# Kernel tuning notes

Measured on AMD Instinct MI355X. Metric: run time of the kernel, lower is better.

## Reference

```python
import jax, jax.numpy as jnp
import numpy as np

N, T = 2000, 8
INFEAT, HID, OUT, H = 32, 16, 32, 4
ALPHA = 0.2
D1 = HID * H   # 64, layer-1 GRU dim (concat heads)
D2 = OUT       # 32, layer-2 GRU dim (mean heads)
NEG = -1e9


def setup_inputs() -> dict:
    key = jax.random.key(0)
    ks = jax.random.split(key, 12)
    xav = lambda k, shape, fi, fo: (jax.random.normal(k, shape, dtype=jnp.float32)
                                    * np.float32(np.sqrt(2.0 / (fi + fo))))
    # sparse-ish binary adjacency with self loops, per timestep
    A = (jax.random.uniform(ks[0], (T, N, N)) < 0.01).astype(jnp.float32)
    A = jnp.maximum(A, jnp.eye(N, dtype=jnp.float32)[None])
    feats = jax.random.normal(ks[1], (T, N, INFEAT), dtype=jnp.float32) * 0.1
    return {
        "A": A,
        "feats": feats,
        "gat1_W": xav(ks[2], (H, INFEAT, HID), INFEAT, HID),
        "gat1_a": xav(ks[3], (H, 2, HID), 2 * HID, 1),
        "gru1_W": xav(ks[4], (3, N, D1, D1), D1, D1),
        "gru1_U": xav(ks[5], (3, N, D1, D1), D1, D1),
        "gru1_b": jnp.zeros((3, N, D1), jnp.float32),
        "q1": xav(ks[6], (N, D1), N, D1),   # GAT_init_features, layer 1
        "gat2_W": xav(ks[7], (H, D1, OUT), D1, OUT),
        "gat2_a": xav(ks[8], (H, 2, OUT), 2 * OUT, 1),
        "gru2_W": xav(ks[9], (3, N, D2, D2), D2, D2),
        "gru2_U": xav(ks[10], (3, N, D2, D2), D2, D2),
        "gru2_b": jnp.zeros((3, N, D2), jnp.float32),
        "q2": xav(ks[11], (N, D2), N, D2),  # GAT_init_features, layer 2
    }


def _gat(x, At, W, a, concat):
    # x: [N,F], At: [N,N], W: [H,F,D], a: [H,2,D]
    h = jnp.einsum('nf,hfd->hnd', x, W)                       # [H,N,D]
    e_src = jnp.einsum('hnd,hd->hn', h, a[:, 0])              # [H,N]
    e_dst = jnp.einsum('hnd,hd->hn', h, a[:, 1])
    e = jax.nn.leaky_relu(e_src[:, :, None] + e_dst[:, None, :], ALPHA)
    e = jnp.where(At[None] > 0, e, NEG)
    att = jax.nn.softmax(e, axis=-1)                          # [H,N,N]
    o = jnp.einsum('hnm,hmd->hnd', att, h)
    if concat:
        return jax.nn.elu(o).transpose(1, 0, 2).reshape(x.shape[0], -1)  # [N,H*D]
    return o.mean(axis=0)                                     # [N,D]


def _gru_step(Q, Z, Wg, Ug, bg):
    # batched per-node mat_GRU_cell: Wg/Ug [3,N,D,D], bg [3,N,D]; gates: update, reset, htilda
    wz = jnp.einsum('gnij,nj->gni', Wg, Z) + bg               # [3,N,D]
    upd = jax.nn.sigmoid(wz[0] + jnp.einsum('nij,nj->ni', Ug[0], Q))
    rst = jax.nn.sigmoid(wz[1] + jnp.einsum('nij,nj->ni', Ug[1], Q))
    hcap = jnp.tanh(wz[2] + jnp.einsum('nij,nj->ni', Ug[2], rst * Q))
    return (1.0 - upd) * Q + upd * hcap


def _grcu_layer(A, feats, q0, W, a, Wg, Ug, bg, concat):
    def step(Q, inp):
        At, xt = inp
        Z = _gat(xt, At, W, a, concat)
        Qn = _gru_step(Q, Z, Wg, Ug, bg)
        return Qn, Qn
    _, seq = jax.lax.scan(step, q0, (A, feats))
    return seq  # [T,N,Dim]


def reference(A, feats, gat1_W, gat1_a, gru1_W, gru1_U, gru1_b, q1,
              gat2_W, gat2_a, gru2_W, gru2_U, gru2_b, q2):
    s1 = _grcu_layer(A, feats, q1, gat1_W, gat1_a, gru1_W, gru1_U, gru1_b, True)
    s2 = _grcu_layer(A, s1, q2, gat2_W, gat2_a, gru2_W, gru2_U, gru2_b, False)
    return s2.reshape(-1, s2.shape[-1])  # torch.cat(out_seq, dim=0) -> [T*N, OUT]
```

## Files before the change

kernel.cpp:

```cpp
#include <hip/hip_runtime.h>
#include <cstdint>
#include <cstddef>

#define NNODES 2000
#define TSTEPS 8
#define NHEADS 4
#define CAP    96
#define NROWS  (TSTEPS * NNODES)

__global__ void k1_csr_gath1(const float* __restrict__ A,
                             int* __restrict__ nbr, int* __restrict__ cnt,
                             const float* __restrict__ feats,
                             const float* __restrict__ W, const float* __restrict__ a,
                             float* __restrict__ hbuf, float* __restrict__ es,
                             float* __restrict__ ed) {
    const int lane = threadIdx.x;
    if (blockIdx.x < NROWS) {
        const int row = blockIdx.x;
        const float4* Ar4 = reinterpret_cast<const float4*>(A + (size_t)row * NNODES);
        int* outp = nbr + (size_t)row * CAP;
        const unsigned long long lmask = (1ull << lane) - 1ull;
        int c = 0;
        for (int j4 = lane; j4 < NNODES / 4; j4 += 64) {
            float4 v = Ar4[j4];
            #pragma unroll
            for (int cc = 0; cc < 4; ++cc) {
                float x = (cc == 0) ? v.x : (cc == 1) ? v.y : (cc == 2) ? v.z : v.w;
                bool p = x > 0.0f;
                unsigned long long m = __ballot(p);
                int off = __popcll(m & lmask);
                if (p && c + off < CAP) outp[c + off] = j4 * 4 + cc;
                c += (int)__popcll(m);
            }
        }
        if (lane == 0) cnt[row] = (c > CAP ? CAP : c);
    } else {
        const int b = blockIdx.x - NROWS;
        const int t = b / NNODES, n = b % NNODES;
        constexpr int F = 32, D = 16;
        const int h = lane / D, d = lane % D;
        const float* xr = feats + (size_t)b * F;
        const float* Wp = W + (size_t)h * F * D + d;
        float acc = 0.f;
        #pragma unroll
        for (int f = 0; f < F; ++f) acc += xr[f] * Wp[f * D];
        hbuf[(((size_t)t * NHEADS + h) * NNODES + n) * D + d] = acc;
        float s0 = acc * a[(h * 2 + 0) * D + d];
        float s1 = acc * a[(h * 2 + 1) * D + d];
        #pragma unroll
        for (int s = D / 2; s > 0; s >>= 1) {
            s0 += __shfl_down(s0, s, D);
            s1 += __shfl_down(s1, s, D);
        }
        if (d == 0) {
            es[((size_t)t * NHEADS + h) * NNODES + n] = s0;
            ed[((size_t)t * NHEADS + h) * NNODES + n] = s1;
        }
    }
}

template<int F, int D>
__global__ void gat_h_all_kernel(const float* __restrict__ x, const float* __restrict__ W,
                                 const float* __restrict__ a, float* __restrict__ hbuf,
                                 float* __restrict__ es, float* __restrict__ ed) {
    const int b = blockIdx.x;
    const int t = b / NNODES, n = b % NNODES;
    const int tid = threadIdx.x;
    const int h = tid / D, d = tid % D;
    const float* xr = x + (size_t)b * F;
    const float* Wp = W + (size_t)h * F * D + d;
    float acc = 0.f;
    #pragma unroll
    for (int f = 0; f < F; ++f) acc += xr[f] * Wp[f * D];
    hbuf[(((size_t)t * NHEADS + h) * NNODES + n) * D + d] = acc;
    float s0 = acc * a[(h * 2 + 0) * D + d];
    float s1 = acc * a[(h * 2 + 1) * D + d];
    #pragma unroll
    for (int s = D / 2; s > 0; s >>= 1) {
        s0 += __shfl_down(s0, s, D);
        s1 += __shfl_down(s1, s, D);
    }
    if (d == 0) {
        es[((size_t)t * NHEADS + h) * NNODES + n] = s0;
        ed[((size_t)t * NHEADS + h) * NNODES + n] = s1;
    }
}

template<int D, bool CONCAT>
__global__ void gat_attn_all_kernel(const int* __restrict__ nbr, const int* __restrict__ cnt_arr,
                                    const float* __restrict__ hbuf, const float* __restrict__ es,
                                    const float* __restrict__ ed, float* __restrict__ Z) {
    const int b = blockIdx.x;
    const int t = b / NNODES, n = b % NNODES;
    const int tid = threadIdx.x;
    const int h = tid / D, d = tid % D;
    const int cnt = cnt_arr[b];
    const int* idx = nbr + (size_t)b * CAP;
    const float* esb = es + (size_t)t * NHEADS * NNODES;
    const float* edb = ed + (size_t)t * NHEADS * NNODES;
    const float* hb  = hbuf + (size_t)t * NHEADS * NNODES * D;
    __shared__ int mlist[CAP];
    __shared__ float eds[NHEADS][CAP];
    for (int k = tid; k < cnt; k += NHEADS * D) mlist[k] = idx[k];
    __syncthreads();
    for (int k = d; k < cnt; k += D) eds[h][k] = edb[(size_t)h * NNODES + mlist[k]];
    __syncthreads();
    const float esv = esb[(size_t)h * NNODES + n];
    float maxv = -1e30f;
    for (int k = 0; k < cnt; ++k) {
        float v = esv + eds[h][k];
        v = v > 0.f ? v : 0.2f * v;
        maxv = fmaxf(maxv, v);
    }
    float wsum = 0.f, acc = 0.f;
    for (int k = 0; k < cnt; ++k) {
        float v = esv + eds[h][k];
        v = v > 0.f ? v : 0.2f * v;
        float w = __expf(v - maxv);
        wsum += w;
        acc += w * hb[((size_t)h * NNODES + mlist[k]) * D + d];
    }
    float o = acc / wsum;
    if constexpr (CONCAT) {
        float e = o > 0.f ? o : (__expf(o) - 1.0f);
        Z[(size_t)b * (NHEADS * D) + h * D + d] = e;
    } else {
        __shared__ float red[NHEADS][D];
        red[h][d] = o;
        __syncthreads();
        if (h == 0) Z[(size_t)b * D + d] =
            (red[0][d] + red[1][d] + red[2][d] + red[3][d]) * 0.25f;
    }
}

template<int D>
__global__ __launch_bounds__((D / 16) * D, 1)
void wzgru_kernel(const float* __restrict__ Wg, const float* __restrict__ Ug,
                  const float* __restrict__ bg, const float* __restrict__ Z,
                  const float* __restrict__ q0, float* __restrict__ outp) {
    constexpr int QUADS = D / 16;
    constexpr int TPB = QUADS * D;
    constexpr int F4R = D / 4;
    const int n = blockIdx.x, tid = threadIdx.x;
    const int quad = tid & (QUADS - 1);
    const int row  = tid / QUADS;
    const int cbase = quad * 16;
    __shared__ float Zs[TSTEPS][D];
    __shared__ float Qs[D], rq[D];

    for (int idx = tid; idx < TSTEPS * F4R; idx += TPB) {
        int t = idx / F4R, i4 = idx % F4R;
        reinterpret_cast<float4*>(&Zs[t][0])[i4] =
            reinterpret_cast<const float4*>(Z + ((size_t)t * NNODES + n) * D)[i4];
    }
    if (tid < D) Qs[tid] = q0[(size_t)n * D + tid];
    float bgv[3];
    #pragma unroll
    for (int g = 0; g < 3; ++g) bgv[g] = bg[((size_t)g * NNODES + n) * D + row];

    float wseg[3][16], useg[3][16];
    #pragma unroll
    for (int g = 0; g < 3; ++g) {
        const float4* W4 = reinterpret_cast<const float4*>(
            Wg + ((size_t)g * NNODES + n) * D * D + (size_t)row * D + cbase);
        #pragma unroll
        for (int c = 0; c < 4; ++c) {
            float4 v = W4[c];
            wseg[g][c * 4 + 0] = v.x; wseg[g][c * 4 + 1] = v.y;
            wseg[g][c * 4 + 2] = v.z; wseg[g][c * 4 + 3] = v.w;
        }
    }
    #pragma unroll
    for (int g = 0; g < 3; ++g) {
        const float4* U4 = reinterpret_cast<const float4*>(
            Ug + ((size_t)g * NNODES + n) * D * D + (size_t)row * D + cbase);
        #pragma unroll
        for (int c = 0; c < 4; ++c) {
            float4 v = U4[c];
            useg[g][c * 4 + 0] = v.x; useg[g][c * 4 + 1] = v.y;
            useg[g][c * 4 + 2] = v.z; useg[g][c * 4 + 3] = v.w;
        }
    }
    __syncthreads();

    float wzr[3][TSTEPS];
    #pragma unroll
    for (int t = 0; t < TSTEPS; ++t) {
        float z16[16];
        #pragma unroll
        for (int c = 0; c < 4; ++c) {
            float4 v = reinterpret_cast<const float4*>(&Zs[t][cbase])[c];
            z16[c * 4 + 0] = v.x; z16[c * 4 + 1] = v.y;
            z16[c * 4 + 2] = v.z; z16[c * 4 + 3] = v.w;
        }
        #pragma unroll
        for (int g = 0; g < 3; ++g) {
            float p = 0.f;
            #pragma unroll
            for (int c = 0; c < 16; ++c) p += wseg[g][c] * z16[c];
            if constexpr (QUADS == 4) { p += __shfl_xor(p, 1, 4); p += __shfl_xor(p, 2, 4); }
            else                      { p += __shfl_xor(p, 1, 2); }
            wzr[g][t] = p + bgv[g];
        }
    }

    #pragma unroll
    for (int t = 0; t < TSTEPS; ++t) {
        float q16[16];
        #pragma unroll
        for (int c = 0; c < 4; ++c) {
            float4 v = reinterpret_cast<const float4*>(&Qs[cbase])[c];
            q16[c * 4 + 0] = v.x; q16[c * 4 + 1] = v.y;
            q16[c * 4 + 2] = v.z; q16[c * 4 + 3] = v.w;
        }
        float p0 = 0.f, p1 = 0.f;
        #pragma unroll
        for (int c = 0; c < 16; ++c) { p0 += useg[0][c] * q16[c]; p1 += useg[1][c] * q16[c]; }
        if constexpr (QUADS == 4) {
            p0 += __shfl_xor(p0, 1, 4); p0 += __shfl_xor(p0, 2, 4);
            p1 += __shfl_xor(p1, 1, 4); p1 += __shfl_xor(p1, 2, 4);
        } else {
            p0 += __shfl_xor(p0, 1, 2); p1 += __shfl_xor(p1, 1, 2);
        }
        const float qrow = Qs[row];
        const float zg = 1.f / (1.f + __expf(-(wzr[0][t] + p0)));
        const float rg = 1.f / (1.f + __expf(-(wzr[1][t] + p1)));
        if (quad == 0) rq[row] = rg * qrow;
        __syncthreads();
        float p2 = 0.f;
        {
            float r16[16];
            #pragma unroll
            for (int c = 0; c < 4; ++c) {
                float4 v = reinterpret_cast<const float4*>(&rq[cbase])[c];
                r16[c * 4 + 0] = v.x; r16[c * 4 + 1] = v.y;
                r16[c * 4 + 2] = v.z; r16[c * 4 + 3] = v.w;
            }
            #pragma unroll
            for (int c = 0; c < 16; ++c) p2 += useg[2][c] * r16[c];
        }
        if constexpr (QUADS == 4) { p2 += __shfl_xor(p2, 1, 4); p2 += __shfl_xor(p2, 2, 4); }
        else                      { p2 += __shfl_xor(p2, 1, 2); }
        const float hcap = tanhf(wzr[2][t] + p2);
        const float qn = (1.f - zg) * qrow + zg * hcap;
        if (quad == 0) {
            Qs[row] = qn;
            outp[((size_t)t * NNODES + n) * D + row] = qn;
        }
        __syncthreads();
    }
}

extern "C" void kernel_launch(void* const* d_in, const int* in_sizes, int n_in,
                              void* d_out, int out_size, void* d_ws, size_t ws_size,
                              hipStream_t stream) {
    const float* A      = (const float*)d_in[0];
    const float* feats  = (const float*)d_in[1];
    const float* gat1_W = (const float*)d_in[2];
    const float* gat1_a = (const float*)d_in[3];
    const float* gru1_W = (const float*)d_in[4];
    const float* gru1_U = (const float*)d_in[5];
    const float* gru1_b = (const float*)d_in[6];
    const float* q1     = (const float*)d_in[7];
    const float* gat2_W = (const float*)d_in[8];
    const float* gat2_a = (const float*)d_in[9];
    const float* gru2_W = (const float*)d_in[10];
    const float* gru2_U = (const float*)d_in[11];
    const float* gru2_b = (const float*)d_in[12];
    const float* q2     = (const float*)d_in[13];
    float* out = (float*)d_out;

    char* ws = (char*)d_ws;
    int*   nbr  = (int*)ws;    ws += (size_t)NROWS * CAP * 4;
    int*   cnt  = (int*)ws;    ws += (size_t)NROWS * 4;
    float* h1   = (float*)ws;  ws += (size_t)TSTEPS * NHEADS * NNODES * 16 * 4;
    float* es1  = (float*)ws;  ws += (size_t)TSTEPS * NHEADS * NNODES * 4;
    float* ed1  = (float*)ws;  ws += (size_t)TSTEPS * NHEADS * NNODES * 4;
    float* Z1   = (float*)ws;  ws += (size_t)TSTEPS * NNODES * 64 * 4;
    float* s1   = (float*)ws;  ws += (size_t)TSTEPS * NNODES * 64 * 4;
    float* h2   = (float*)ws;  ws += (size_t)TSTEPS * NHEADS * NNODES * 32 * 4;
    float* es2  = (float*)ws;  ws += (size_t)TSTEPS * NHEADS * NNODES * 4;
    float* ed2  = (float*)ws;  ws += (size_t)TSTEPS * NHEADS * NNODES * 4;
    float* Z2   = (float*)ws;  ws += (size_t)TSTEPS * NNODES * 32 * 4;

    k1_csr_gath1<<<2 * NROWS, 64, 0, stream>>>(A, nbr, cnt, feats, gat1_W, gat1_a,
                                               h1, es1, ed1);
    gat_attn_all_kernel<16, true><<<NROWS, 64, 0, stream>>>(nbr, cnt, h1, es1, ed1, Z1);
    wzgru_kernel<64><<<NNODES, 256, 0, stream>>>(gru1_W, gru1_U, gru1_b, Z1, q1, s1);
    gat_h_all_kernel<64, 32><<<NROWS, 128, 0, stream>>>(s1, gat2_W, gat2_a, h2, es2, ed2);
    gat_attn_all_kernel<32, false><<<NROWS, 128, 0, stream>>>(nbr, cnt, h2, es2, ed2, Z2);
    wzgru_kernel<32><<<NNODES, 64, 0, stream>>>(gru2_W, gru2_U, gru2_b, Z2, q2, out);
}
```

Baseline: 173.9 us.

## Fuse layer-1 GRU with layer-2 GAT feature projection into one kernel

The layer-1 GRU kernel now also keeps each node's hidden states for all timesteps in shared memory. It then computes the layer-2 GAT projection h2 and the attention scores es2/ed2 directly from them. This removes the s1 intermediate buffer round-trip through global memory and one kernel launch of 16000 blocks. In exchange the fused kernel holds the W2 slice in more registers, and its projection work runs over only 2000 blocks of 256 threads.

New measurement: 166.3 us. 1.05x faster.

```diff
diff --git a/kernel.cpp b/kernel.cpp
--- a/kernel.cpp
+++ b/kernel.cpp
@@ -56,33 +56,6 @@
             es[((size_t)t * NHEADS + h) * NNODES + n] = s0;
             ed[((size_t)t * NHEADS + h) * NNODES + n] = s1;
         }
-    }
-}
-
-template<int F, int D>
-__global__ void gat_h_all_kernel(const float* __restrict__ x, const float* __restrict__ W,
-                                 const float* __restrict__ a, float* __restrict__ hbuf,
-                                 float* __restrict__ es, float* __restrict__ ed) {
-    const int b = blockIdx.x;
-    const int t = b / NNODES, n = b % NNODES;
-    const int tid = threadIdx.x;
-    const int h = tid / D, d = tid % D;
-    const float* xr = x + (size_t)b * F;
-    const float* Wp = W + (size_t)h * F * D + d;
-    float acc = 0.f;
-    #pragma unroll
-    for (int f = 0; f < F; ++f) acc += xr[f] * Wp[f * D];
-    hbuf[(((size_t)t * NHEADS + h) * NNODES + n) * D + d] = acc;
-    float s0 = acc * a[(h * 2 + 0) * D + d];
-    float s1 = acc * a[(h * 2 + 1) * D + d];
-    #pragma unroll
-    for (int s = D / 2; s > 0; s >>= 1) {
-        s0 += __shfl_down(s0, s, D);
-        s1 += __shfl_down(s1, s, D);
-    }
-    if (d == 0) {
-        es[((size_t)t * NHEADS + h) * NNODES + n] = s0;
-        ed[((size_t)t * NHEADS + h) * NNODES + n] = s1;
     }
 }
 
@@ -133,6 +106,152 @@
     }
 }
 
+__global__ __launch_bounds__(256, 1)
+void wzgru1_gath2_kernel(const float* __restrict__ Wg, const float* __restrict__ Ug,
+                         const float* __restrict__ bg, const float* __restrict__ Z,
+                         const float* __restrict__ q0,
+                         const float* __restrict__ W2, const float* __restrict__ a2,
+                         float* __restrict__ h2, float* __restrict__ es2,
+                         float* __restrict__ ed2) {
+    constexpr int D = 64;
+    constexpr int QUADS = 4;
+    constexpr int TPB = 256;
+    constexpr int F4R = D / 4;
+    const int n = blockIdx.x, tid = threadIdx.x;
+    const int quad = tid & (QUADS - 1);
+    const int row  = tid / QUADS;
+    const int cbase = quad * 16;
+    __shared__ float Zs[TSTEPS][D];
+    __shared__ float Qh[TSTEPS][D];
+    __shared__ float Qs[D], rq[D];
+
+    for (int idx = tid; idx < TSTEPS * F4R; idx += TPB) {
+        int t = idx / F4R, i4 = idx % F4R;
+        reinterpret_cast<float4*>(&Zs[t][0])[i4] =
+            reinterpret_cast<const float4*>(Z + ((size_t)t * NNODES + n) * D)[i4];
+    }
+    if (tid < D) Qs[tid] = q0[(size_t)n * D + tid];
+    float bgv[3];
+    #pragma unroll
+    for (int g = 0; g < 3; ++g) bgv[g] = bg[((size_t)g * NNODES + n) * D + row];
+
+    float wseg[3][16], useg[3][16];
+    #pragma unroll
+    for (int g = 0; g < 3; ++g) {
+        const float4* W4 = reinterpret_cast<const float4*>(
+            Wg + ((size_t)g * NNODES + n) * D * D + (size_t)row * D + cbase);
+        #pragma unroll
+        for (int c = 0; c < 4; ++c) {
+            float4 v = W4[c];
+            wseg[g][c * 4 + 0] = v.x; wseg[g][c * 4 + 1] = v.y;
+            wseg[g][c * 4 + 2] = v.z; wseg[g][c * 4 + 3] = v.w;
+        }
+    }
+    #pragma unroll
+    for (int g = 0; g < 3; ++g) {
+        const float4* U4 = reinterpret_cast<const float4*>(
+            Ug + ((size_t)g * NNODES + n) * D * D + (size_t)row * D + cbase);
+        #pragma unroll
+        for (int c = 0; c < 4; ++c) {
+            float4 v = U4[c];
+            useg[g][c * 4 + 0] = v.x; useg[g][c * 4 + 1] = v.y;
+            useg[g][c * 4 + 2] = v.z; useg[g][c * 4 + 3] = v.w;
+        }
+    }
+    __syncthreads();
+
+    float wzr[3][TSTEPS];
+    #pragma unroll
+    for (int t = 0; t < TSTEPS; ++t) {
+        float z16[16];
+        #pragma unroll
+        for (int c = 0; c < 4; ++c) {
+            float4 v = reinterpret_cast<const float4*>(&Zs[t][cbase])[c];
+            z16[c * 4 + 0] = v.x; z16[c * 4 + 1] = v.y;
+            z16[c * 4 + 2] = v.z; z16[c * 4 + 3] = v.w;
+        }
+        #pragma unroll
+        for (int g = 0; g < 3; ++g) {
+            float p = 0.f;
+            #pragma unroll
+            for (int c = 0; c < 16; ++c) p += wseg[g][c] * z16[c];
+            p += __shfl_xor(p, 1, 4); p += __shfl_xor(p, 2, 4);
+            wzr[g][t] = p + bgv[g];
+        }
+    }
+
+    #pragma unroll
+    for (int t = 0; t < TSTEPS; ++t) {
+        float q16[16];
+        #pragma unroll
+        for (int c = 0; c < 4; ++c) {
+            float4 v = reinterpret_cast<const float4*>(&Qs[cbase])[c];
+            q16[c * 4 + 0] = v.x; q16[c * 4 + 1] = v.y;
+            q16[c * 4 + 2] = v.z; q16[c * 4 + 3] = v.w;
+        }
+        float p0 = 0.f, p1 = 0.f;
+        #pragma unroll
+        for (int c = 0; c < 16; ++c) { p0 += useg[0][c] * q16[c]; p1 += useg[1][c] * q16[c]; }
+        p0 += __shfl_xor(p0, 1, 4); p0 += __shfl_xor(p0, 2, 4);
+        p1 += __shfl_xor(p1, 1, 4); p1 += __shfl_xor(p1, 2, 4);
+        const float qrow = Qs[row];
+        const float zg = 1.f / (1.f + __expf(-(wzr[0][t] + p0)));
+        const float rg = 1.f / (1.f + __expf(-(wzr[1][t] + p1)));
+        if (quad == 0) rq[row] = rg * qrow;
+        __syncthreads();
+        float p2 = 0.f;
+        {
+            float r16[16];
+            #pragma unroll
+            for (int c = 0; c < 4; ++c) {
+                float4 v = reinterpret_cast<const float4*>(&rq[cbase])[c];
+                r16[c * 4 + 0] = v.x; r16[c * 4 + 1] = v.y;
+                r16[c * 4 + 2] = v.z; r16[c * 4 + 3] = v.w;
+            }
+            #pragma unroll
+            for (int c = 0; c < 16; ++c) p2 += useg[2][c] * r16[c];
+        }
+        p2 += __shfl_xor(p2, 1, 4); p2 += __shfl_xor(p2, 2, 4);
+        const float hcap = tanhf(wzr[2][t] + p2);
+        const float qn = (1.f - zg) * qrow + zg * hcap;
+        if (quad == 0) {
+            Qs[row] = qn;
+            Qh[t][row] = qn;
+        }
+        __syncthreads();
+    }
+
+    const int lane = tid & 63;
+    const int hh = tid >> 6;
+    const int d2 = lane >> 1;
+    const int fh = lane & 1;
+    float w2seg[32];
+    const float* W2p = W2 + ((size_t)hh * 64 + fh * 32) * 32 + d2;
+    #pragma unroll
+    for (int j = 0; j < 32; ++j) w2seg[j] = W2p[(size_t)j * 32];
+    const float a0 = a2[(hh * 2 + 0) * 32 + d2];
+    const float a1 = a2[(hh * 2 + 1) * 32 + d2];
+    #pragma unroll
+    for (int t = 0; t < TSTEPS; ++t) {
+        float p = 0.f;
+        #pragma unroll
+        for (int j = 0; j < 32; ++j) p += w2seg[j] * Qh[t][fh * 32 + j];
+        p += __shfl_xor(p, 1, 64);
+        if (fh == 0) h2[(((size_t)t * NHEADS + hh) * NNODES + n) * 32 + d2] = p;
+        float e0 = (fh == 0) ? p * a0 : 0.f;
+        float e1 = (fh == 0) ? p * a1 : 0.f;
+        #pragma unroll
+        for (int s = 2; s <= 32; s <<= 1) {
+            e0 += __shfl_xor(e0, s, 64);
+            e1 += __shfl_xor(e1, s, 64);
+        }
+        if (lane == 0) {
+            es2[((size_t)t * NHEADS + hh) * NNODES + n] = e0;
+            ed2[((size_t)t * NHEADS + hh) * NNODES + n] = e1;
+        }
+    }
+}
+
 template<int D>
 __global__ __launch_bounds__((D / 16) * D, 1)
 void wzgru_kernel(const float* __restrict__ Wg, const float* __restrict__ Ug,
@@ -277,7 +396,6 @@
     float* es1  = (float*)ws;  ws += (size_t)TSTEPS * NHEADS * NNODES * 4;
     float* ed1  = (float*)ws;  ws += (size_t)TSTEPS * NHEADS * NNODES * 4;
     float* Z1   = (float*)ws;  ws += (size_t)TSTEPS * NNODES * 64 * 4;
-    float* s1   = (float*)ws;  ws += (size_t)TSTEPS * NNODES * 64 * 4;
     float* h2   = (float*)ws;  ws += (size_t)TSTEPS * NHEADS * NNODES * 32 * 4;
     float* es2  = (float*)ws;  ws += (size_t)TSTEPS * NHEADS * NNODES * 4;
     float* ed2  = (float*)ws;  ws += (size_t)TSTEPS * NHEADS * NNODES * 4;
@@ -286,8 +404,8 @@
     k1_csr_gath1<<<2 * NROWS, 64, 0, stream>>>(A, nbr, cnt, feats, gat1_W, gat1_a,
                                                h1, es1, ed1);
     gat_attn_all_kernel<16, true><<<NROWS, 64, 0, stream>>>(nbr, cnt, h1, es1, ed1, Z1);
-    wzgru_kernel<64><<<NNODES, 256, 0, stream>>>(gru1_W, gru1_U, gru1_b, Z1, q1, s1);
-    gat_h_all_kernel<64, 32><<<NROWS, 128, 0, stream>>>(s1, gat2_W, gat2_a, h2, es2, ed2);
+    wzgru1_gath2_kernel<<<NNODES, 256, 0, stream>>>(gru1_W, gru1_U, gru1_b, Z1, q1,
+                                                    gat2_W, gat2_a, h2, es2, ed2);
     gat_attn_all_kernel<32, false><<<NROWS, 128, 0, stream>>>(nbr, cnt, h2, es2, ed2, Z2);
     wzgru_kernel<32><<<NNODES, 64, 0, stream>>>(gru2_W, gru2_U, gru2_b, Z2, q2, out);
 }
```

## Fuse layer-1 GRU with layer-2 GAT projection and use row-per-thread GRU

Applied to the files above, without the earlier changes.

Merges the layer-1 GRU recurrence and the layer-2 GAT projection and score computation into one kernel. The GRU state for each timestep stays in shared memory instead of being written to and reread from a global s1 buffer, and one kernel launch is removed. Both GRU kernels now give each thread a full weight row (64 or 32 columns held in registers) instead of splitting rows across 4 or 2 threads with shuffle reductions. The layer-2 GRU packs two nodes into each 64-thread block. The trade is much higher register pressure (192+ floats per thread for U) and fewer threads per node, which lowers latency hiding when streaming the weights.

After: 192.5 us. 1.11x slower.

```diff
diff --git a/kernel.cpp b/kernel.cpp
--- a/kernel.cpp
+++ b/kernel.cpp
@@ -59,33 +59,6 @@
     }
 }
 
-template<int F, int D>
-__global__ void gat_h_all_kernel(const float* __restrict__ x, const float* __restrict__ W,
-                                 const float* __restrict__ a, float* __restrict__ hbuf,
-                                 float* __restrict__ es, float* __restrict__ ed) {
-    const int b = blockIdx.x;
-    const int t = b / NNODES, n = b % NNODES;
-    const int tid = threadIdx.x;
-    const int h = tid / D, d = tid % D;
-    const float* xr = x + (size_t)b * F;
-    const float* Wp = W + (size_t)h * F * D + d;
-    float acc = 0.f;
-    #pragma unroll
-    for (int f = 0; f < F; ++f) acc += xr[f] * Wp[f * D];
-    hbuf[(((size_t)t * NHEADS + h) * NNODES + n) * D + d] = acc;
-    float s0 = acc * a[(h * 2 + 0) * D + d];
-    float s1 = acc * a[(h * 2 + 1) * D + d];
-    #pragma unroll
-    for (int s = D / 2; s > 0; s >>= 1) {
-        s0 += __shfl_down(s0, s, D);
-        s1 += __shfl_down(s1, s, D);
-    }
-    if (d == 0) {
-        es[((size_t)t * NHEADS + h) * NNODES + n] = s0;
-        ed[((size_t)t * NHEADS + h) * NNODES + n] = s1;
-    }
-}
-
 template<int D, bool CONCAT>
 __global__ void gat_attn_all_kernel(const int* __restrict__ nbr, const int* __restrict__ cnt_arr,
                                     const float* __restrict__ hbuf, const float* __restrict__ es,
@@ -133,120 +106,244 @@
     }
 }
 
-template<int D>
-__global__ __launch_bounds__((D / 16) * D, 1)
-void wzgru_kernel(const float* __restrict__ Wg, const float* __restrict__ Ug,
-                  const float* __restrict__ bg, const float* __restrict__ Z,
-                  const float* __restrict__ q0, float* __restrict__ outp) {
-    constexpr int QUADS = D / 16;
-    constexpr int TPB = QUADS * D;
-    constexpr int F4R = D / 4;
-    const int n = blockIdx.x, tid = threadIdx.x;
-    const int quad = tid & (QUADS - 1);
-    const int row  = tid / QUADS;
-    const int cbase = quad * 16;
+__global__ __launch_bounds__(64, 1)
+void wzgru1_gath2_kernel(const float* __restrict__ Wg, const float* __restrict__ Ug,
+                         const float* __restrict__ bg, const float* __restrict__ Z,
+                         const float* __restrict__ q0,
+                         const float* __restrict__ W2, const float* __restrict__ a2,
+                         float* __restrict__ h2, float* __restrict__ es2,
+                         float* __restrict__ ed2) {
+    constexpr int D = 64;
+    const int n = blockIdx.x;
+    const int r = threadIdx.x;
     __shared__ float Zs[TSTEPS][D];
-    __shared__ float Qs[D], rq[D];
-
-    for (int idx = tid; idx < TSTEPS * F4R; idx += TPB) {
-        int t = idx / F4R, i4 = idx % F4R;
+    __shared__ float wzl[3][TSTEPS][D];
+    __shared__ float Qh[TSTEPS][D];
+    __shared__ float Qs[D], rqs[D];
+
+    for (int i = r; i < TSTEPS * 16; i += 64) {
+        int t = i / 16, i4 = i % 16;
         reinterpret_cast<float4*>(&Zs[t][0])[i4] =
             reinterpret_cast<const float4*>(Z + ((size_t)t * NNODES + n) * D)[i4];
     }
-    if (tid < D) Qs[tid] = q0[(size_t)n * D + tid];
-    float bgv[3];
-    #pragma unroll
-    for (int g = 0; g < 3; ++g) bgv[g] = bg[((size_t)g * NNODES + n) * D + row];
-
-    float wseg[3][16], useg[3][16];
-    #pragma unroll
+    Qs[r] = q0[(size_t)n * D + r];
+    __syncthreads();
+
     for (int g = 0; g < 3; ++g) {
+        float wrow[64];
         const float4* W4 = reinterpret_cast<const float4*>(
-            Wg + ((size_t)g * NNODES + n) * D * D + (size_t)row * D + cbase);
-        #pragma unroll
-        for (int c = 0; c < 4; ++c) {
+            Wg + ((size_t)g * NNODES + n) * D * D) + (size_t)r * 16;
+        #pragma unroll
+        for (int c = 0; c < 16; ++c) {
             float4 v = W4[c];
-            wseg[g][c * 4 + 0] = v.x; wseg[g][c * 4 + 1] = v.y;
-            wseg[g][c * 4 + 2] = v.z; wseg[g][c * 4 + 3] = v.w;
-        }
-    }
+            wrow[c * 4 + 0] = v.x; wrow[c * 4 + 1] = v.y;
+            wrow[c * 4 + 2] = v.z; wrow[c * 4 + 3] = v.w;
+        }
+        const float bgv = bg[((size_t)g * NNODES + n) * D + r];
+        for (int t = 0; t < TSTEPS; ++t) {
+            const float4* Z4 = reinterpret_cast<const float4*>(&Zs[t][0]);
+            float acc[4] = {0.f, 0.f, 0.f, 0.f};
+            #pragma unroll
+            for (int c = 0; c < 16; ++c) {
+                float4 v = Z4[c];
+                acc[c & 3] += wrow[c * 4 + 0] * v.x + wrow[c * 4 + 1] * v.y
+                            + wrow[c * 4 + 2] * v.z + wrow[c * 4 + 3] * v.w;
+            }
+            wzl[g][t][r] = ((acc[0] + acc[1]) + (acc[2] + acc[3])) + bgv;
+        }
+    }
+
+    float useg[3][64];
     #pragma unroll
     for (int g = 0; g < 3; ++g) {
         const float4* U4 = reinterpret_cast<const float4*>(
-            Ug + ((size_t)g * NNODES + n) * D * D + (size_t)row * D + cbase);
-        #pragma unroll
-        for (int c = 0; c < 4; ++c) {
+            Ug + ((size_t)g * NNODES + n) * D * D) + (size_t)r * 16;
+        #pragma unroll
+        for (int c = 0; c < 16; ++c) {
             float4 v = U4[c];
             useg[g][c * 4 + 0] = v.x; useg[g][c * 4 + 1] = v.y;
             useg[g][c * 4 + 2] = v.z; useg[g][c * 4 + 3] = v.w;
         }
     }
-    __syncthreads();
-
-    float wzr[3][TSTEPS];
-    #pragma unroll
+    #pragma unroll
+    for (int g = 0; g < 3; ++g)
+        #pragma unroll
+        for (int c = 0; c < 64; ++c) asm volatile("" : "+v"(useg[g][c]));
+    __syncthreads();
+
     for (int t = 0; t < TSTEPS; ++t) {
-        float z16[16];
-        #pragma unroll
-        for (int c = 0; c < 4; ++c) {
-            float4 v = reinterpret_cast<const float4*>(&Zs[t][cbase])[c];
-            z16[c * 4 + 0] = v.x; z16[c * 4 + 1] = v.y;
-            z16[c * 4 + 2] = v.z; z16[c * 4 + 3] = v.w;
-        }
-        #pragma unroll
-        for (int g = 0; g < 3; ++g) {
-            float p = 0.f;
+        const float4* Q4 = reinterpret_cast<const float4*>(Qs);
+        float ua[4] = {0.f, 0.f, 0.f, 0.f}, ub[4] = {0.f, 0.f, 0.f, 0.f};
+        #pragma unroll
+        for (int c = 0; c < 16; ++c) {
+            float4 v = Q4[c];
+            ua[c & 3] += useg[0][c * 4 + 0] * v.x + useg[0][c * 4 + 1] * v.y
+                       + useg[0][c * 4 + 2] * v.z + useg[0][c * 4 + 3] * v.w;
+            ub[c & 3] += useg[1][c * 4 + 0] * v.x + useg[1][c * 4 + 1] * v.y
+                       + useg[1][c * 4 + 2] * v.z + useg[1][c * 4 + 3] * v.w;
+        }
+        const float p0 = (ua[0] + ua[1]) + (ua[2] + ua[3]);
+        const float p1 = (ub[0] + ub[1]) + (ub[2] + ub[3]);
+        const float qrow = Qs[r];
+        const float zg = 1.f / (1.f + __expf(-(wzl[0][t][r] + p0)));
+        const float rg = 1.f / (1.f + __expf(-(wzl[1][t][r] + p1)));
+        rqs[r] = rg * qrow;
+        __syncthreads();
+        const float4* R4 = reinterpret_cast<const float4*>(rqs);
+        float uc[4] = {0.f, 0.f, 0.f, 0.f};
+        #pragma unroll
+        for (int c = 0; c < 16; ++c) {
+            float4 v = R4[c];
+            uc[c & 3] += useg[2][c * 4 + 0] * v.x + useg[2][c * 4 + 1] * v.y
+                       + useg[2][c * 4 + 2] * v.z + useg[2][c * 4 + 3] * v.w;
+        }
+        const float p2 = (uc[0] + uc[1]) + (uc[2] + uc[3]);
+        const float hcap = tanhf(wzl[2][t][r] + p2);
+        const float qn = (1.f - zg) * qrow + zg * hcap;
+        __syncthreads();
+        Qs[r] = qn;
+        Qh[t][r] = qn;
+        __syncthreads();
+    }
+
+    const int half = r >> 5, d2 = r & 31;
+    float w2a[64], w2b[64];
+    #pragma unroll
+    for (int j = 0; j < 64; ++j) {
+        w2a[j] = W2[((size_t)half * 64 + j) * 32 + d2];
+        w2b[j] = W2[((size_t)(half + 2) * 64 + j) * 32 + d2];
+    }
+    const float a0A = a2[(half * 2 + 0) * 32 + d2];
+    const float a1A = a2[(half * 2 + 1) * 32 + d2];
+    const float a0B = a2[((half + 2) * 2 + 0) * 32 + d2];
+    const float a1B = a2[((half + 2) * 2 + 1) * 32 + d2];
+    for (int t = 0; t < TSTEPS; ++t) {
+        const float4* Qt4 = reinterpret_cast<const float4*>(&Qh[t][0]);
+        float pa[4] = {0.f, 0.f, 0.f, 0.f}, pb[4] = {0.f, 0.f, 0.f, 0.f};
+        #pragma unroll
+        for (int c = 0; c < 16; ++c) {
+            float4 v = Qt4[c];
+            pa[c & 3] += w2a[c * 4 + 0] * v.x + w2a[c * 4 + 1] * v.y
+                       + w2a[c * 4 + 2] * v.z + w2a[c * 4 + 3] * v.w;
+            pb[c & 3] += w2b[c * 4 + 0] * v.x + w2b[c * 4 + 1] * v.y
+                       + w2b[c * 4 + 2] * v.z + w2b[c * 4 + 3] * v.w;
+        }
+        const float pA = (pa[0] + pa[1]) + (pa[2] + pa[3]);
+        const float pB = (pb[0] + pb[1]) + (pb[2] + pb[3]);
+        h2[(((size_t)t * NHEADS + half) * NNODES + n) * 32 + d2] = pA;
+        h2[(((size_t)t * NHEADS + half + 2) * NNODES + n) * 32 + d2] = pB;
+        float e0A = pA * a0A, e1A = pA * a1A, e0B = pB * a0B, e1B = pB * a1B;
+        #pragma unroll
+        for (int s = 1; s <= 16; s <<= 1) {
+            e0A += __shfl_xor(e0A, s, 64); e1A += __shfl_xor(e1A, s, 64);
+            e0B += __shfl_xor(e0B, s, 64); e1B += __shfl_xor(e1B, s, 64);
+        }
+        if (d2 == 0) {
+            es2[((size_t)t * NHEADS + half) * NNODES + n]     = e0A;
+            ed2[((size_t)t * NHEADS + half) * NNODES + n]     = e1A;
+            es2[((size_t)t * NHEADS + half + 2) * NNODES + n] = e0B;
+            ed2[((size_t)t * NHEADS + half + 2) * NNODES + n] = e1B;
+        }
+    }
+}
+
+__global__ __launch_bounds__(64, 1)
+void wzgru2_kernel(const float* __restrict__ Wg, const float* __restrict__ Ug,
+                   const float* __restrict__ bg, const float* __restrict__ Z,
+                   const float* __restrict__ q0, float* __restrict__ outp) {
+    constexpr int D = 32;
+    const int tid = threadIdx.x;
+    const int nh = tid >> 5;
+    const int r  = tid & 31;
+    const int n = blockIdx.x * 2 + nh;
+    __shared__ float Zs[2][TSTEPS][D];
+    __shared__ float wzl[2][3][TSTEPS][D];
+    __shared__ float Qs[2][D], rqs[2][D];
+
+    for (int i = tid; i < 2 * TSTEPS * 8; i += 64) {
+        int node_h = i / (TSTEPS * 8), rem = i % (TSTEPS * 8);
+        int t = rem / 8, i4 = rem % 8;
+        reinterpret_cast<float4*>(&Zs[node_h][t][0])[i4] =
+            reinterpret_cast<const float4*>(
+                Z + ((size_t)t * NNODES + blockIdx.x * 2 + node_h) * D)[i4];
+    }
+    Qs[nh][r] = q0[(size_t)n * D + r];
+    __syncthreads();
+
+    for (int g = 0; g < 3; ++g) {
+        float wrow[32];
+        const float4* W4 = reinterpret_cast<const float4*>(
+            Wg + ((size_t)g * NNODES + n) * D * D) + (size_t)r * 8;
+        #pragma unroll
+        for (int c = 0; c < 8; ++c) {
+            float4 v = W4[c];
+            wrow[c * 4 + 0] = v.x; wrow[c * 4 + 1] = v.y;
+            wrow[c * 4 + 2] = v.z; wrow[c * 4 + 3] = v.w;
+        }
+        const float bgv = bg[((size_t)g * NNODES + n) * D + r];
+        for (int t = 0; t < TSTEPS; ++t) {
+            const float4* Z4 = reinterpret_cast<const float4*>(&Zs[nh][t][0]);
+            float acc[4] = {0.f, 0.f, 0.f, 0.f};
             #pragma unroll
-            for (int c = 0; c < 16; ++c) p += wseg[g][c] * z16[c];
-            if constexpr (QUADS == 4) { p += __shfl_xor(p, 1, 4); p += __shfl_xor(p, 2, 4); }
-            else                      { p += __shfl_xor(p, 1, 2); }
-            wzr[g][t] = p + bgv[g];
-        }
-    }
-
-    #pragma unroll
+            for (int c = 0; c < 8; ++c) {
+                float4 v = Z4[c];
+                acc[c & 3] += wrow[c * 4 + 0] * v.x + wrow[c * 4 + 1] * v.y
+                            + wrow[c * 4 + 2] * v.z + wrow[c * 4 + 3] * v.w;
+            }
+            wzl[nh][g][t][r] = ((acc[0] + acc[1]) + (acc[2] + acc[3])) + bgv;
+        }
+    }
+
+    float useg[3][32];
+    #pragma unroll
+    for (int g = 0; g < 3; ++g) {
+        const float4* U4 = reinterpret_cast<const float4*>(
+            Ug + ((size_t)g * NNODES + n) * D * D) + (size_t)r * 8;
+        #pragma unroll
+        for (int c = 0; c < 8; ++c) {
+            float4 v = U4[c];
+            useg[g][c * 4 + 0] = v.x; useg[g][c * 4 + 1] = v.y;
+            useg[g][c * 4 + 2] = v.z; useg[g][c * 4 + 3] = v.w;
+        }
+    }
+    #pragma unroll
+    for (int g = 0; g < 3; ++g)
+        #pragma unroll
+        for (int c = 0; c < 32; ++c) asm volatile("" : "+v"(useg[g][c]));
+    __syncthreads();
+
     for (int t = 0; t < TSTEPS; ++t) {
-        float q16[16];
-        #pragma unroll
-        for (int c = 0; c < 4; ++c) {
-            float4 v = reinterpret_cast<const float4*>(&Qs[cbase])[c];
-            q16[c * 4 + 0] = v.x; q16[c * 4 + 1] = v.y;
-            q16[c * 4 + 2] = v.z; q16[c * 4 + 3] = v.w;
-        }
-        float p0 = 0.f, p1 = 0.f;
-        #pragma unroll
-        for (int c = 0; c < 16; ++c) { p0 += useg[0][c] * q16[c]; p1 += useg[1][c] * q16[c]; }
-        if constexpr (QUADS == 4) {
-            p0 += __shfl_xor(p0, 1, 4); p0 += __shfl_xor(p0, 2, 4);
-            p1 += __shfl_xor(p1, 1, 4); p1 += __shfl_xor(p1, 2, 4);
-        } else {
-            p0 += __shfl_xor(p0, 1, 2); p1 += __shfl_xor(p1, 1, 2);
-        }
-        const float qrow = Qs[row];
-        const float zg = 1.f / (1.f + __expf(-(wzr[0][t] + p0)));
-        const float rg = 1.f / (1.f + __expf(-(wzr[1][t] + p1)));
-        if (quad == 0) rq[row] = rg * qrow;
-        __syncthreads();
-        float p2 = 0.f;
-        {
-            float r16[16];
-            #pragma unroll
-            for (int c = 0; c < 4; ++c) {
-                float4 v = reinterpret_cast<const float4*>(&rq[cbase])[c];
-                r16[c * 4 + 0] = v.x; r16[c * 4 + 1] = v.y;
-                r16[c * 4 + 2] = v.z; r16[c * 4 + 3] = v.w;
-            }
-            #pragma unroll
-            for (int c = 0; c < 16; ++c) p2 += useg[2][c] * r16[c];
-        }
-        if constexpr (QUADS == 4) { p2 += __shfl_xor(p2, 1, 4); p2 += __shfl_xor(p2, 2, 4); }
-        else                      { p2 += __shfl_xor(p2, 1, 2); }
-        const float hcap = tanhf(wzr[2][t] + p2);
+        const float4* Q4 = reinterpret_cast<const float4*>(&Qs[nh][0]);
+        float ua[4] = {0.f, 0.f, 0.f, 0.f}, ub[4] = {0.f, 0.f, 0.f, 0.f};
+        #pragma unroll
+        for (int c = 0; c < 8; ++c) {
+            float4 v = Q4[c];
+            ua[c & 3] += useg[0][c * 4 + 0] * v.x + useg[0][c * 4 + 1] * v.y
+                       + useg[0][c * 4 + 2] * v.z + useg[0][c * 4 + 3] * v.w;
+            ub[c & 3] += useg[1][c * 4 + 0] * v.x + useg[1][c * 4 + 1] * v.y
+                       + useg[1][c * 4 + 2] * v.z + useg[1][c * 4 + 3] * v.w;
+        }
+        const float p0 = (ua[0] + ua[1]) + (ua[2] + ua[3]);
+        const float p1 = (ub[0] + ub[1]) + (ub[2] + ub[3]);
+        const float qrow = Qs[nh][r];
+        const float zg = 1.f / (1.f + __expf(-(wzl[nh][0][t][r] + p0)));
+        const float rg = 1.f / (1.f + __expf(-(wzl[nh][1][t][r] + p1)));
+        rqs[nh][r] = rg * qrow;
+        __syncthreads();
+        const float4* R4 = reinterpret_cast<const float4*>(&rqs[nh][0]);
+        float uc[4] = {0.f, 0.f, 0.f, 0.f};
+        #pragma unroll
+        for (int c = 0; c < 8; ++c) {
+            float4 v = R4[c];
+            uc[c & 3] += useg[2][c * 4 + 0] * v.x + useg[2][c * 4 + 1] * v.y
+                       + useg[2][c * 4 + 2] * v.z + useg[2][c * 4 + 3] * v.w;
+        }
+        const float p2 = (uc[0] + uc[1]) + (uc[2] + uc[3]);
+        const float hcap = tanhf(wzl[nh][2][t][r] + p2);
         const float qn = (1.f - zg) * qrow + zg * hcap;
-        if (quad == 0) {
-            Qs[row] = qn;
-            outp[((size_t)t * NNODES + n) * D + row] = qn;
-        }
+        __syncthreads();
+        Qs[nh][r] = qn;
+        outp[((size_t)t * NNODES + n) * D + r] = qn;
         __syncthreads();
     }
 }
@@ -277,7 +374,6 @@
     float* es1  = (float*)ws;  ws += (size_t)TSTEPS * NHEADS * NNODES * 4;
     float* ed1  = (float*)ws;  ws += (size_t)TSTEPS * NHEADS * NNODES * 4;
     float* Z1   = (float*)ws;  ws += (size_t)TSTEPS * NNODES * 64 * 4;
-    float* s1   = (float*)ws;  ws += (size_t)TSTEPS * NNODES * 64 * 4;
     float* h2   = (float*)ws;  ws += (size_t)TSTEPS * NHEADS * NNODES * 32 * 4;
     float* es2  = (float*)ws;  ws += (size_t)TSTEPS * NHEADS * NNODES * 4;
     float* ed2  = (float*)ws;  ws += (size_t)TSTEPS * NHEADS * NNODES * 4;
@@ -286,8 +382,8 @@
     k1_csr_gath1<<<2 * NROWS, 64, 0, stream>>>(A, nbr, cnt, feats, gat1_W, gat1_a,
                                                h1, es1, ed1);
     gat_attn_all_kernel<16, true><<<NROWS, 64, 0, stream>>>(nbr, cnt, h1, es1, ed1, Z1);
-    wzgru_kernel<64><<<NNODES, 256, 0, stream>>>(gru1_W, gru1_U, gru1_b, Z1, q1, s1);
-    gat_h_all_kernel<64, 32><<<NROWS, 128, 0, stream>>>(s1, gat2_W, gat2_a, h2, es2, ed2);
+    wzgru1_gath2_kernel<<<NNODES, 64, 0, stream>>>(gru1_W, gru1_U, gru1_b, Z1, q1,
+                                                   gat2_W, gat2_a, h2, es2, ed2);
     gat_attn_all_kernel<32, false><<<NROWS, 128, 0, stream>>>(nbr, cnt, h2, es2, ed2, Z2);
-    wzgru_kernel<32><<<NNODES, 64, 0, stream>>>(gru2_W, gru2_U, gru2_b, Z2, q2, out);
-}
+    wzgru2_kernel<<<NNODES / 2, 64, 0, stream>>>(gru2_W, gru2_U, gru2_b, Z2, q2, out);
+}
```
